# Performance work log

Measured on AMD Instinct MI355X. Metric: run time of the kernel, lower is better.

The kernel has to match this reference:

```python
import jax, jax.numpy as jnp
import numpy as np
from jax import lax

CORR = 5        # patch_size of correlation (5x5 displacements)
PAD = (CORR - 1) // 2
SEQ_IDS = [0, 1, 3, 4]  # gating_seq_len=5, center frame index 2 is skipped


def conv2d(x, w, b):
    # 3x3, stride 1, padding 1 == SAME; NCHW / OIHW
    y = lax.conv_general_dilated(x, w, (1, 1), 'SAME',
                                 dimension_numbers=('NCHW', 'OIHW', 'NCHW'))
    return y + b[None, :, None, None]


def _xavier(k, shape):
    fan_in = shape[1] * shape[2] * shape[3]
    fan_out = shape[0] * shape[2] * shape[3]
    limit = float(np.sqrt(6.0 / (fan_in + fan_out)))
    return jax.random.uniform(k, shape, jnp.float32, -limit, limit)


def setup_inputs() -> dict:
    key = jax.random.key(0)
    ks = jax.random.split(key, 4)
    B, C, H, W = 2, 512, 64, 64
    x = jax.random.normal(ks[0], (5, B, C, H, W), jnp.float32)
    Wg = jnp.stack([_xavier(k, (2, 2 * C, 3, 3)) for k in jax.random.split(ks[1], 4)])
    bg = jnp.zeros((4, 2), jnp.float32)
    Wd = jnp.stack([_xavier(k, (C, 2 * C, 3, 3)) for k in jax.random.split(ks[2], 4)])
    bd = jnp.zeros((4, C), jnp.float32)
    Wc = _xavier(ks[3], (C, 4 * C, 3, 3))
    bc = jnp.zeros((C,), jnp.float32)
    return dict(x=x, Wg=Wg, bg=bg, Wd=Wd, bd=bd, Wc=Wc, bc=bc)


def _align(feat2, feat1):
    # spatial_correlation_sample(feat2, feat1, kernel=1, patch=5, pad=0):
    # corr[b, d, y, x] = sum_c feat2[b,c,y,x] * feat1[b,c,y+di,x+dj], di,dj in [-2,2]
    b, c, h, w = feat1.shape
    pad1 = jnp.pad(feat1, ((0, 0), (0, 0), (PAD, PAD), (PAD, PAD)))
    corr = jnp.stack([jnp.sum(feat2 * pad1[:, :, i:i + h, j:j + w], axis=1)
                      for i in range(CORR) for j in range(CORR)], axis=1)  # [b,25,h,w]
    # torch F.softmax default dim for 4D is dim=1; scaled by 20/global-max
    attn = jax.nn.softmax(corr * (20.0 / jnp.max(corr)), axis=1)
    # shifted-window weighted sum over the 25 displacements
    new_feat = jnp.zeros_like(feat1)
    for i in range(CORR):
        for j in range(CORR):
            new_feat = new_feat + attn[:, i * CORR + j][:, None] * pad1[:, :, i:i + h, j:j + w]
    return new_feat


def reference(x, Wg, bg, Wd, bd, Wc, bc):
    center = x[2]                       # feat2 = middle frame for every pair
    C = center.shape[1]
    gated = []
    for n, s in enumerate(SEQ_IDS):
        new_feat = _align(center, x[s])
        feat = jnp.concatenate([center, new_feat], axis=1)          # [B,2C,H,W]
        gw = jax.nn.sigmoid(conv2d(feat, Wg[n], bg[n]))              # [B,2,H,W]
        fg = jnp.concatenate([center * gw[:, 0:1], new_feat * gw[:, 1:2]], axis=1)
        gated.append(jax.nn.relu(conv2d(fg, Wd[n], bd[n])))          # [B,C,H,W]
    total = jnp.concatenate(gated, axis=1)                           # [B,4C,H,W]
    return jax.nn.relu(conv2d(total, Wc, bc))
```

## Files before the change

### kernel.cpp

```cpp
#include <hip/hip_runtime.h>
#include <hip/hip_bf16.h>
#include <stdint.h>

typedef __attribute__((ext_vector_type(8))) short bf16x8;
typedef __attribute__((ext_vector_type(4))) float f32x4;
typedef __attribute__((ext_vector_type(2))) float f32x2;
typedef __attribute__((ext_vector_type(4))) int int4v;

#define DEVI static __device__ __forceinline__

DEVI unsigned short f2b(float f) {
  union { float f; unsigned u; } v; v.f = f;
  unsigned r = (v.u + 0x7FFFu + ((v.u >> 16) & 1u)) >> 16;
  return (unsigned short)r;
}
DEVI float b2f(unsigned short h) {
  union { unsigned u; float f; } v; v.u = ((unsigned)h) << 16;
  return v.f;
}
DEVI unsigned encf(float f) {
  union { float f; unsigned u; } v; v.f = f;
  return (v.u & 0x80000000u) ? ~v.u : (v.u | 0x80000000u);
}
DEVI float decf(unsigned u) {
  union { unsigned u; float f; } v;
  v.u = (u & 0x80000000u) ? (u & 0x7FFFFFFFu) : ~u;
  return v.f;
}
DEVI void gload16(const void* g, void* l) {
  __builtin_amdgcn_global_load_lds(
      (const __attribute__((address_space(1))) unsigned int*)g,
      (__attribute__((address_space(3))) unsigned int*)l, 16, 0, 0);
}

__global__ __launch_bounds__(256) void k_reorder_w2(const float* __restrict__ src,
                                                    unsigned short* __restrict__ dst,
                                                    int CI) {
  int r = blockIdx.x;
  int t = threadIdx.x;
  const float* s = src + (size_t)r * CI * 9;
  unsigned short* d = dst + (size_t)r * CI * 9;
  for (int ci0 = 0; ci0 < CI; ci0 += 256) {
    int ci = ci0 + t;
    float v[9];
#pragma unroll
    for (int k = 0; k < 9; k++) v[k] = s[(size_t)ci * 9 + k];
    unsigned short* db = d + (size_t)(ci >> 5) * 288 + (ci & 31);
#pragma unroll
    for (int k = 0; k < 9; k++) db[(size_t)k * 32] = f2b(v[k]);
  }
}

__global__ void k_reorder_wg(const float* __restrict__ src, float* __restrict__ dst) {
  int idx = blockIdx.x * 256 + threadIdx.x;
  int ci = idx & 1023;
  int rt = idx >> 10;
  int tap = rt % 9;
  int po = rt / 9;
  dst[(((size_t)po * 9 + tap) * 32 + (ci & 31)) * 32 + (ci >> 5)] =
      src[((size_t)po * 1024 + ci) * 9 + tap];
}

__global__ void k_border(unsigned short* __restrict__ p, int H, int wpad, int C8,
                         int nImg) {
  int inner = H - 2 * wpad;
  int borderPx = H * H - inner * inner;
  long total = (long)borderPx * C8 * nImg;
  int topN = wpad * H;
  for (long i = (long)blockIdx.x * 256 + threadIdx.x; i < total;
       i += (long)gridDim.x * 256) {
    int c = (int)(i % C8);
    long r2 = i / C8;
    int px = (int)(r2 % borderPx);
    int img = (int)(r2 / borderPx);
    int y, x;
    if (px < topN) {
      y = px / H; x = px % H;
    } else if (px < 2 * topN) {
      int q = px - topN; y = H - 1 - (q / H); x = q % H;
    } else {
      int q = px - 2 * topN;
      int row = q / (2 * wpad), cc = q % (2 * wpad);
      y = wpad + row;
      x = cc < wpad ? cc : H - 2 * wpad + cc;
    }
    *(int4v*)&p[((((size_t)img * H + y) * H + x) * C8 + c) * 8] = int4v{0, 0, 0, 0};
  }
}

__global__ __launch_bounds__(256) void k_pad(const float* __restrict__ xin,
                                             unsigned short* __restrict__ xf1,
                                             unsigned short* __restrict__ cp) {
  __shared__ unsigned short lds[64 * 66];
  int t = threadIdx.x;
  int y = blockIdx.x;
  int fb = blockIdx.y;
  int f = fb >> 1, b = fb & 1;
  const float* src = xin + (size_t)fb * 512 * 4096 + y * 64;
  unsigned short* base;
  if (f == 2) {
    base = cp + (((size_t)b * 66) + y + 1) * 66 * 512 + 512;
  } else {
    int fi = f < 2 ? f : f - 1;
    base = xf1 + (((size_t)(fi * 2 + b) * 68) + y + 2) * 68 * 512 + 2 * 512;
  }
  for (int c0 = 0; c0 < 512; c0 += 64) {
#pragma unroll
    for (int r = 0; r < 16; ++r) {
      int ci = r * 4 + (t >> 6);
      int xx = t & 63;
      lds[ci * 66 + xx] = f2b(src[(size_t)(c0 + ci) * 4096 + xx]);
    }
    __syncthreads();
    int xp = t >> 2;
    int cc = (t & 3) * 16;
    __align__(16) unsigned short vals[16];
#pragma unroll
    for (int i = 0; i < 16; i++) vals[i] = lds[(cc + i) * 66 + xp];
    unsigned short* dst = base + (size_t)xp * 512 + c0 + cc;
    *(int4v*)(dst) = *(const int4v*)(vals);
    *(int4v*)(dst + 8) = *(const int4v*)(vals + 8);
    __syncthreads();
  }
}

__global__ __launch_bounds__(256) void k_corr(const float* __restrict__ xin,
                                              float* __restrict__ corrpart) {
  __shared__ f32x2 f1h2[420];
  int t = threadIdx.x;
  int tx = t & 15, ty = t >> 4;
  int x0 = blockIdx.x * 16, y0 = blockIdx.y * 16;
  int z = blockIdx.z;
  int b = z & 1, pair = (z >> 1) & 3, part = z >> 3;
  int s = pair < 2 ? pair : pair + 1;
  const float* f2 = xin + ((size_t)(2 * 2 + b) * 512) * 4096;
  const float* f1 = xin + ((size_t)(s * 2 + b) * 512) * 4096;

  int r0 = t / 20, c0 = t - r0 * 20;
  int ls0 = r0 * 21 + c0;
  int gy0 = y0 + r0 - 2, gx0 = x0 + c0 - 2;
  bool val0 = ((unsigned)gy0 < 64u) && ((unsigned)gx0 < 64u);
  int go0 = gy0 * 64 + gx0;
  bool has1 = t < 144;
  int s1 = t + 256;
  int r1 = s1 / 20, c1 = s1 - r1 * 20;
  int ls1 = r1 * 21 + c1;
  int gy1 = y0 + r1 - 2, gx1 = x0 + c1 - 2;
  bool val1 = ((unsigned)gy1 < 64u) && ((unsigned)gx1 < 64u);
  int go1 = gy1 * 64 + gx1;

  float acc[25];
#pragma unroll
  for (int d = 0; d < 25; d++) acc[d] = 0.f;
  int y = y0 + ty, x = x0 + tx;
  for (int c = part * 128; c < part * 128 + 128; c += 2) {
    {
      float a0 = 0.f, b0v = 0.f;
      if (val0) {
        a0 = f1[(size_t)c * 4096 + go0];
        b0v = f1[(size_t)(c + 1) * 4096 + go0];
      }
      f1h2[ls0] = f32x2{a0, b0v};
      if (has1) {
        float a1 = 0.f, b1v = 0.f;
        if (val1) {
          a1 = f1[(size_t)c * 4096 + go1];
          b1v = f1[(size_t)(c + 1) * 4096 + go1];
        }
        f1h2[ls1] = f32x2{a1, b1v};
      }
    }
    float f2a = f2[(size_t)c * 4096 + y * 64 + x];
    float f2c = f2[(size_t)(c + 1) * 4096 + y * 64 + x];
    __syncthreads();
#pragma unroll
    for (int d = 0; d < 25; ++d) {
      int di = d / 5, dj = d % 5;
      f32x2 v = f1h2[(ty + di) * 21 + tx + dj];
      acc[d] += f2a * v[0] + f2c * v[1];
    }
    __syncthreads();
  }
  float* out = corrpart + ((size_t)((part * 4 + pair) * 2 + b) * 25) * 4096;
#pragma unroll
  for (int d = 0; d < 25; d++) out[(size_t)d * 4096 + y * 64 + x] = acc[d];
}

__global__ __launch_bounds__(256) void k_corr_combine(const float* __restrict__ cpart,
                                                      float* __restrict__ corr,
                                                      unsigned* __restrict__ maxb) {
  const size_t PERPAIR = (size_t)2 * 25 * 4096;
  int pair = blockIdx.y;
  size_t i4 = ((size_t)blockIdx.x * 256 + threadIdx.x) * 4;
  f32x4 sacc = {0.f, 0.f, 0.f, 0.f};
#pragma unroll
  for (int p = 0; p < 4; p++)
    sacc += *(const f32x4*)(cpart + ((size_t)(p * 4 + pair)) * PERPAIR + i4);
  *(f32x4*)(corr + (size_t)pair * PERPAIR + i4) = sacc;
  float m = fmaxf(fmaxf(sacc[0], sacc[1]), fmaxf(sacc[2], sacc[3]));
#pragma unroll
  for (int off = 32; off; off >>= 1) m = fmaxf(m, __shfl_xor(m, off));
  __shared__ float wm[4];
  if ((threadIdx.x & 63) == 0) wm[threadIdx.x >> 6] = m;
  __syncthreads();
  if (threadIdx.x == 0) {
    float mm = fmaxf(fmaxf(wm[0], wm[1]), fmaxf(wm[2], wm[3]));
    atomicMax(maxb + pair, encf(mm));
  }
}

__global__ __launch_bounds__(256) void k_attn3(const unsigned short* __restrict__ xf1,
                                               const float* __restrict__ corr,
                                               const unsigned* __restrict__ maxb,
                                               unsigned short* __restrict__ nfpad) {
  __shared__ unsigned short f1t[400 * 8];
  int t = threadIdx.x;
  int tx = t & 15, ty = t >> 4;
  int x0 = blockIdx.x * 16, y0 = blockIdx.y * 16;
  int z = blockIdx.z;
  int b = z & 1, pair = (z >> 1) & 3, cgh = z >> 3;
  const unsigned short* f1 = xf1 + ((size_t)(pair * 2 + b)) * 68 * 68 * 512;
  int y = y0 + ty, x = x0 + tx;
  const float* cr = corr + ((size_t)(pair * 2 + b)) * 25 * 4096 + y * 64 + x;

  int r0 = t / 20, c0 = t - r0 * 20;
  size_t go0 = ((size_t)(y0 + r0) * 68 + (x0 + c0)) * 512;
  bool has1 = t < 144;
  int k1 = t + 256;
  int r1 = k1 / 20, c1 = k1 - r1 * 20;
  size_t go1 = ((size_t)(y0 + r1) * 68 + (x0 + c1)) * 512;

  float p[25];
  float mx = -1e30f;
#pragma unroll
  for (int d = 0; d < 25; d++) {
    p[d] = cr[(size_t)d * 4096];
    mx = fmaxf(mx, p[d]);
  }
  float gs = 20.f / decf(maxb[pair]);
  float ss = 0.f;
#pragma unroll
  for (int d = 0; d < 25; d++) {
    p[d] = __expf((p[d] - mx) * gs);
    ss += p[d];
  }
  float inv = 1.f / ss;
#pragma unroll
  for (int d = 0; d < 25; d++) p[d] *= inv;

  for (int q = 0; q < 4; ++q) {
    int cg = cgh * 4 + q;
    *(int4v*)&f1t[t * 8] = *(const int4v*)&f1[go0 + cg * 8];
    if (has1) *(int4v*)&f1t[k1 * 8] = *(const int4v*)&f1[go1 + cg * 8];
    __syncthreads();
    float acc[8] = {0.f, 0.f, 0.f, 0.f, 0.f, 0.f, 0.f, 0.f};
#pragma unroll
    for (int d = 0; d < 25; d++) {
      bf16x8 v = *(const bf16x8*)&f1t[((ty + d / 5) * 20 + tx + d % 5) * 8];
      float pd = p[d];
#pragma unroll
      for (int e = 0; e < 8; e++) acc[e] += pd * b2f((unsigned short)v[e]);
    }
    __align__(16) unsigned short o[8];
#pragma unroll
    for (int e = 0; e < 8; e++) o[e] = f2b(acc[e]);
    *(int4v*)&nfpad[(((size_t)(pair * 2 + b) * 66 + (y + 1)) * 66 + (x + 1)) * 512 +
                    cg * 8] = *(const int4v*)o;
    __syncthreads();
  }
}

__global__ __launch_bounds__(256) void k_gate3(const unsigned short* __restrict__ cp,
                                               const unsigned short* __restrict__ nfp,
                                               const float* __restrict__ wgt,
                                               const float* __restrict__ bg,
                                               float* __restrict__ gw) {
  int t = threadIdx.x;
  int z = blockIdx.z;
  int b = z & 1, pair = z >> 1;
  int y = blockIdx.y;
  int x = blockIdx.x * 8 + (t >> 5);
  int chunk = t & 31;
  int ci0 = chunk * 32;
  int half = ci0 >> 9;
  int ch0 = ci0 & 511;
  const unsigned short* src = half ? (nfp + ((size_t)(pair * 2 + b)) * 66 * 66 * 512)
                                   : (cp + ((size_t)b) * 66 * 66 * 512);
  const float* w0b = wgt + ((size_t)(pair * 2 + 0) * 9) * 1024;
  const float* w1b = wgt + ((size_t)(pair * 2 + 1) * 9) * 1024;
  float a0 = 0.f, a1 = 0.f;
  for (int tap = 0; tap < 9; ++tap) {
    int ky = tap / 3, kx = tap % 3;
    const unsigned short* ip = src + ((size_t)(y + ky) * 66 + (x + kx)) * 512 + ch0;
    const float* w0 = w0b + tap * 1024 + chunk;
    const float* w1 = w1b + tap * 1024 + chunk;
#pragma unroll
    for (int q = 0; q < 4; ++q) {
      bf16x8 v8 = *(const bf16x8*)(ip + q * 8);
#pragma unroll
      for (int e = 0; e < 8; e++) {
        float f = b2f((unsigned short)v8[e]);
        a0 += f * w0[(q * 8 + e) * 32];
        a1 += f * w1[(q * 8 + e) * 32];
      }
    }
  }
#pragma unroll
  for (int md = 1; md < 32; md <<= 1) {
    a0 += __shfl_xor(a0, md);
    a1 += __shfl_xor(a1, md);
  }
  if ((t & 31) == 0) {
    float g0 = 1.f / (1.f + __expf(-(a0 + bg[pair * 2 + 0])));
    float g1 = 1.f / (1.f + __expf(-(a1 + bg[pair * 2 + 1])));
    gw[(((size_t)(pair * 2 + b) * 2 + 0) * 64 + y) * 64 + x] = g0;
    gw[(((size_t)(pair * 2 + b) * 2 + 1) * 64 + y) * 64 + x] = g1;
  }
}

__global__ __launch_bounds__(256) void k_fg(const unsigned short* __restrict__ cp,
                                            const unsigned short* __restrict__ nfp,
                                            const float* __restrict__ gw,
                                            unsigned short* __restrict__ fgp, int pairBase) {
  int pz = blockIdx.y;
  int pair = pairBase + pz;
  unsigned short* dstBase = fgp + (size_t)pz * 2 * 66 * 66 * 1024;
  size_t idx = (size_t)blockIdx.x * 256 + threadIdx.x;
  int chunk = (int)(idx & 127);
  size_t px = idx >> 7;
  int b = (int)(px >> 12), rem = (int)(px & 4095);
  int y = rem >> 6, x = rem & 63;
  int ci0 = chunk * 8;
  int half = ci0 >> 9;
  float g = gw[(((size_t)(pair * 2 + b) * 2 + half) * 64 + y) * 64 + x];
  const unsigned short* src = half ? (nfp + ((size_t)(pair * 2 + b)) * 66 * 66 * 512)
                                   : (cp + (size_t)b * 66 * 66 * 512);
  size_t poff = ((size_t)(y + 1) * 66 + (x + 1)) * 512 + (ci0 - half * 512);
  bf16x8 v = *(const bf16x8*)(src + poff);
  __align__(16) unsigned short o[8];
#pragma unroll
  for (int e = 0; e < 8; e++) o[e] = f2b(b2f((unsigned short)v[e]) * g);
  *(int4v*)(dstBase + ((size_t)(b * 66 + y + 1) * 66 + (x + 1)) * 1024 + ci0) =
      *(const int4v*)o;
}

template <int CI, int MODE>
__global__ __launch_bounds__(512) void conv5(const unsigned short* __restrict__ inB,
                                             const unsigned short* __restrict__ WTb,
                                             const float* __restrict__ bias,
                                             unsigned short* __restrict__ outB,
                                             unsigned short* __restrict__ outP,
                                             int pairOfs, int multiz, int nz) {
  constexpr int K = 9 * CI;
  constexpr int KTOT = K / 64;
  __shared__ unsigned short As[2 * 2 * 8192];
  __shared__ unsigned short Bs[2 * 2 * 8192];

  int t = threadIdx.x;
  int bid = blockIdx.x;
  int z, m, n;
  if (multiz == 2) {
    z = bid & 7; m = (bid >> 3) & 1; n = bid >> 4;
  } else if (multiz == 1) {
    int xcd = bid & 7;
    z = xcd >> 1; m = xcd & 1; n = bid >> 3;
  } else {
    z = 0; m = bid & 1; n = bid >> 1;
  }
  const int KT = (MODE == 2) ? KTOT / nz : KTOT;
  const unsigned short* inPad = (MODE == 0) ? inB + (size_t)z * 2 * 66 * 66 * 1024 : inB;
  const unsigned short* WT = (MODE == 0) ? WTb + (size_t)z * 512 * 9216 : WTb;
  const int kt0 = (MODE == 2) ? z * KT : 0;
  const int ktEnd = kt0 + KT;
  int co0 = m * 256, n0 = n * 256;

  int rowS[2], kcS[2], linS[2];
  size_t bpix2[2][2];
#pragma unroll
  for (int rr = 0; rr < 2; rr++) {
    int idx2 = rr * 512 + t;
    rowS[rr] = idx2 >> 3;
    kcS[rr] = (idx2 & 7) ^ (rowS[rr] & 7);
    linS[rr] = idx2 * 8;
#pragma unroll
    for (int h = 0; h < 2; h++) {
      int ng = n0 + h * 128 + rowS[rr];
      int bb = ng >> 12, yy = (ng >> 6) & 63, xx = ng & 63;
      bpix2[h][rr] = (size_t)((bb * 66 + yy) * 66 + xx) * CI + (kcS[rr] & 3) * 8;
    }
  }

  f32x4 acc[8][4];
#pragma unroll
  for (int i = 0; i < 8; i++)
#pragma unroll
    for (int j = 0; j < 4; j++) acc[i][j] = f32x4{0.f, 0.f, 0.f, 0.f};

  int wid = t >> 6, l = t & 63;
  int wm = wid >> 2, wn = wid & 3;
  int lrow = l & 15, lk4 = l >> 4;

  auto stA = [&](int bufp, int h, int kt) {
#pragma unroll
    for (int rr = 0; rr < 2; rr++)
      gload16(WT + (size_t)(co0 + h * 128 + rowS[rr]) * K + kt * 64 + kcS[rr] * 8,
              &As[(bufp * 2 + h) * 8192 + linS[rr]]);
  };
  auto stB = [&](int bufp, int h, int kt) {
    int g0 = kt * 2, g1 = g0 + 1;
    int cib0 = g0 / 9, tap0 = g0 - cib0 * 9;
    int cib1 = g1 / 9, tap1 = g1 - cib1 * 9;
    int off0 = ((tap0 / 3) * 66 + tap0 % 3) * CI + cib0 * 32;
    int off1 = ((tap1 / 3) * 66 + tap1 % 3) * CI + cib1 * 32;
#pragma unroll
    for (int rr = 0; rr < 2; rr++)
      gload16(inPad + bpix2[h][rr] + ((kcS[rr] & 4) ? off1 : off0),
              &Bs[(bufp * 2 + h) * 8192 + linS[rr]]);
  };

  bf16x8 afr0[4][2], afr1[4][2], bfr0[2][2], bfr1[2][2];

#define RDA(DST, C, MH)                                                         \
  _Pragma("unroll") for (int ii = 0; ii < 4; ++ii) {                            \
    int row = (MH)*64 + ii * 16 + lrow;                                         \
    _Pragma("unroll") for (int kk = 0; kk < 2; ++kk) {                          \
      int pos = (kk * 4 + lk4) ^ (lrow & 7);                                    \
      DST[ii][kk] = *(const bf16x8*)&As[((C)*2 + wm) * 8192 + row * 64 + pos * 8]; \
    }                                                                           \
  }
#define RDB(DST, C, NH)                                                         \
  _Pragma("unroll") for (int j = 0; j < 2; ++j) {                               \
    int row = (wn & 1) * 64 + (NH)*32 + j * 16 + lrow;                          \
    _Pragma("unroll") for (int kk = 0; kk < 2; ++kk) {                          \
      int pos = (kk * 4 + lk4) ^ (lrow & 7);                                    \
      DST[j][kk] =                                                              \
          *(const bf16x8*)&Bs[((C)*2 + (wn >> 1)) * 8192 + row * 64 + pos * 8]; \
    }                                                                           \
  }
#define QUAD(AF, BF, MH, NH)                                                    \
  __builtin_amdgcn_s_setprio(1);                                                \
  _Pragma("unroll") for (int ii = 0; ii < 4; ++ii) {                            \
    _Pragma("unroll") for (int j = 0; j < 2; ++j) {                             \
      _Pragma("unroll") for (int kk = 0; kk < 2; ++kk) {                        \
        acc[(MH)*4 + ii][(NH)*2 + j] = __builtin_amdgcn_mfma_f32_16x16x32_bf16( \
            AF[ii][kk], BF[j][kk], acc[(MH)*4 + ii][(NH)*2 + j], 0, 0, 0);      \
      }                                                                         \
    }                                                                           \
  }                                                                             \
  __builtin_amdgcn_s_setprio(0);
#define DRAIN_LGKM asm volatile("s_waitcnt lgkmcnt(0)" ::: "memory");

  {
    int b0 = kt0 & 1, b1 = b0 ^ 1;
    stA(b0, 0, kt0); stA(b0, 1, kt0); stB(b0, 0, kt0); stB(b0, 1, kt0);
    stA(b1, 0, kt0 + 1); stA(b1, 1, kt0 + 1); stB(b1, 0, kt0 + 1); stB(b1, 1, kt0 + 1);
    asm volatile("s_waitcnt vmcnt(8)" ::: "memory");
    __builtin_amdgcn_s_barrier();
  }

  for (int kt = kt0; kt < ktEnd; ++kt) {
    int cur = kt & 1;
    const bool pf = (kt + 2 < ktEnd);
    RDA(afr0, cur, 0);
    RDB(bfr0, cur, 0);
    QUAD(afr0, bfr0, 0, 0)
    RDA(afr1, cur, 1);
    QUAD(afr1, bfr0, 1, 0)
    DRAIN_LGKM
    __builtin_amdgcn_s_barrier();
    if (pf) { stA(cur, 0, kt + 2); stA(cur, 1, kt + 2); }
    RDB(bfr1, cur, 1);
    QUAD(afr1, bfr1, 1, 1)
    DRAIN_LGKM
    __builtin_amdgcn_s_barrier();
    if (pf) { stB(cur, 0, kt + 2); stB(cur, 1, kt + 2); }
    QUAD(afr0, bfr1, 0, 1)
    if (pf) {
      asm volatile("s_waitcnt vmcnt(8)" ::: "memory");
    } else {
      asm volatile("s_waitcnt vmcnt(0)" ::: "memory");
    }
    __builtin_amdgcn_s_barrier();
  }
#undef RDA
#undef RDB
#undef QUAD
#undef DRAIN_LGKM

#pragma unroll
  for (int i = 0; i < 8; i++) {
#pragma unroll
    for (int j = 0; j < 4; j++) {
      int col = wn * 64 + j * 16 + lrow;
      int ng = n0 + col;
      int bb = ng >> 12, yy = (ng >> 6) & 63, xx = ng & 63;
#pragma unroll
      for (int r = 0; r < 4; r++) {
        int row = wm * 128 + i * 16 + lk4 * 4 + r;
        int co = co0 + row;
        if (MODE == 0) {
          int zc = (z + pairOfs) * 512 + co;
          float v = acc[i][j][r] + bias[zc];
          v = v > 0.f ? v : 0.f;
          outB[((size_t)(bb * 66 + yy + 1) * 66 + (xx + 1)) * 2048 + zc] = f2b(v);
        } else {
          outP[((size_t)(z * 512 + co) << 13) + ng] = f2b(acc[i][j][r]);
        }
      }
    }
  }
}

__global__ __launch_bounds__(256) void k_combine2(const unsigned short* __restrict__ p,
                                                  const float* __restrict__ bc,
                                                  float* __restrict__ out, int nz) {
  size_t i8 = ((size_t)blockIdx.x * 256 + threadIdx.x) * 8;
  int co = (int)(i8 >> 13);
  int ng = (int)(i8 & 8191);
  float s[8] = {0.f, 0.f, 0.f, 0.f, 0.f, 0.f, 0.f, 0.f};
  for (int zz = 0; zz < nz; zz++) {
    bf16x8 v = *(const bf16x8*)&p[((size_t)(zz * 512 + co) << 13) + ng];
#pragma unroll
    for (int e = 0; e < 8; e++) s[e] += b2f((unsigned short)v[e]);
  }
  float bb = bc[co];
  int batch = ng >> 12, rem = ng & 4095;
  float* o = out + (((size_t)(batch * 512 + co)) << 12) + rem;
#pragma unroll
  for (int e = 0; e < 8; e++) {
    float q = s[e] + bb;
    o[e] = q > 0.f ? q : 0.f;
  }
}

extern "C" void kernel_launch(void* const* d_in, const int* in_sizes, int n_in,
                              void* d_out, int out_size, void* d_ws, size_t ws_size,
                              hipStream_t stream) {
  const float* x = (const float*)d_in[0];
  const float* Wg = (const float*)d_in[1];
  const float* bg = (const float*)d_in[2];
  const float* Wd = (const float*)d_in[3];
  const float* bd = (const float*)d_in[4];
  const float* Wc = (const float*)d_in[5];
  const float* bc = (const float*)d_in[6];
  float* out = (float*)d_out;

  char* ws = (char*)d_ws;
  size_t off = 0;
  auto alloc = [&](size_t bytes) {
    void* p = ws + off;
    off = (off + bytes + 255) & ~(size_t)255;
    return p;
  };
  const size_t SZ_WDT = (size_t)2048 * 9216 * 2;
  const size_t SZ_WCT = (size_t)512 * 18432 * 2;
  const size_t SZ_WGT = (size_t)4 * 2 * 9 * 1024 * 4;
  const size_t SZ_CP = (size_t)2 * 66 * 66 * 512 * 2;
  const size_t SZ_NF = (size_t)4 * 2 * 66 * 66 * 512 * 2;
  const size_t SZ_GT = (size_t)2 * 66 * 66 * 2048 * 2;
  const size_t SZ_GW = (size_t)4 * 2 * 2 * 4096 * 4;
  const size_t SZ_XF1 = (size_t)4 * 2 * 68 * 68 * 512 * 2;
  const size_t SZ_CORR = (size_t)4 * 2 * 25 * 4096 * 4;
  const size_t SZ_FG1 = (size_t)2 * 66 * 66 * 1024 * 2;
  const size_t SZ_FG4 = SZ_FG1 * 4;

  unsigned short* WdT = (unsigned short*)alloc(SZ_WDT);
  unsigned short* WcT = (unsigned short*)alloc(SZ_WCT);
  float* WgT = (float*)alloc(SZ_WGT);
  unsigned short* centerpad = (unsigned short*)alloc(SZ_CP);
  unsigned short* nfpad = (unsigned short*)alloc(SZ_NF);
  unsigned short* gatedpad = (unsigned short*)alloc(SZ_GT);
  float* gw = (float*)alloc(SZ_GW);
  unsigned* maxb = (unsigned*)alloc(256);

  size_t unionOff = off;
  unsigned short* xf1 = (unsigned short*)(ws + unionOff);
  size_t o2 = unionOff + ((SZ_XF1 + 255) & ~(size_t)255);
  float* corr = (float*)(ws + o2);
  float* cpart = (float*)(ws + o2 + ((SZ_CORR + 255) & ~(size_t)255));
  unsigned short* fg = (unsigned short*)(ws + unionOff);
  unsigned short* wcp = (unsigned short*)(ws + unionOff);
  bool batched = ws_size >= unionOff + SZ_FG4;

  hipMemsetAsync(maxb, 0, 64, stream);

  k_border<<<512, 256, 0, stream>>>(xf1, 68, 2, 64, 8);
  k_border<<<512, 256, 0, stream>>>(centerpad, 66, 1, 64, 2);
  k_border<<<512, 256, 0, stream>>>(nfpad, 66, 1, 64, 8);
  k_border<<<512, 256, 0, stream>>>(gatedpad, 66, 1, 256, 2);

  k_reorder_w2<<<2048, 256, 0, stream>>>(Wd, WdT, 1024);
  k_reorder_w2<<<512, 256, 0, stream>>>(Wc, WcT, 2048);
  k_reorder_wg<<<288, 256, 0, stream>>>(Wg, WgT);
  k_pad<<<dim3(64, 10), 256, 0, stream>>>(x, xf1, centerpad);
  k_corr<<<dim3(4, 4, 32), 256, 0, stream>>>(x, cpart);
  k_corr_combine<<<dim3(200, 4), 256, 0, stream>>>(cpart, corr, maxb);
  k_attn3<<<dim3(4, 4, 128), 256, 0, stream>>>(xf1, corr, maxb, nfpad);
  k_gate3<<<dim3(8, 64, 8), 256, 0, stream>>>(centerpad, nfpad, WgT, bg, gw);

  k_border<<<512, 256, 0, stream>>>(fg, 66, 1, 128, batched ? 8 : 2);

  if (batched) {
    k_fg<<<dim3(4096, 4), 256, 0, stream>>>(centerpad, nfpad, gw, fg, 0);
    conv5<1024, 0><<<256, 512, 0, stream>>>(fg, WdT, bd, gatedpad, nullptr, 0, 1, 1);
    conv5<2048, 2><<<512, 512, 0, stream>>>(gatedpad, WcT, nullptr, nullptr, wcp, 0, 2, 8);
    k_combine2<<<2048, 256, 0, stream>>>(wcp, bc, out, 8);
  } else {
    for (int pair = 0; pair < 4; ++pair) {
      k_fg<<<dim3(4096, 1), 256, 0, stream>>>(centerpad, nfpad, gw, fg, pair);
      conv5<1024, 0><<<64, 512, 0, stream>>>(
          fg, WdT + (size_t)pair * 512 * 9216, bd, gatedpad, nullptr, pair, 0, 1);
    }
    conv5<2048, 2><<<256, 512, 0, stream>>>(gatedpad, WcT, nullptr, nullptr, wcp, 0, 1, 4);
    k_combine2<<<2048, 256, 0, stream>>>(wcp, bc, out, 4);
  }
}
```

Measured before the change: 757.9 us.

## Shrink conv GEMM tiles to 128x128x32 with 256-thread blocks for more occupancy

Replaces the 256x256x64 tile conv kernel (512 threads, 128KB LDS) with a 128x128x32 tile variant using 256 threads and launch bounds allowing 4 blocks per CU. The smaller LDS and register footprint lets several blocks share a CU, and the launch adds many more blocks for better load balance. Split-K for the final conv is reduced (8 to 4 batched, 4 to 2 unbatched), which shrinks the partial-sum traffic. In exchange, each byte loaded gets less reuse and there are more global loads per FLOP.

```diff
diff --git a/kernel.cpp b/kernel.cpp
--- a/kernel.cpp
+++ b/kernel.cpp
@@ -345,116 +345,108 @@
 }
 
 template <int CI, int MODE>
-__global__ __launch_bounds__(512) void conv5(const unsigned short* __restrict__ inB,
-                                             const unsigned short* __restrict__ WTb,
-                                             const float* __restrict__ bias,
-                                             unsigned short* __restrict__ outB,
-                                             unsigned short* __restrict__ outP,
-                                             int pairOfs, int multiz, int nz) {
+__global__ __launch_bounds__(256, 4) void conv8(const unsigned short* __restrict__ inB,
+                                                const unsigned short* __restrict__ WTb,
+                                                const float* __restrict__ bias,
+                                                unsigned short* __restrict__ outB,
+                                                unsigned short* __restrict__ outP,
+                                                int pairOfs, int multiz, int nzLog) {
   constexpr int K = 9 * CI;
-  constexpr int KTOT = K / 64;
-  __shared__ unsigned short As[2 * 2 * 8192];
-  __shared__ unsigned short Bs[2 * 2 * 8192];
+  constexpr int KTOT = K / 32;
+  __shared__ unsigned short As[2 * 4096];
+  __shared__ unsigned short Bs[2 * 4096];
 
   int t = threadIdx.x;
   int bid = blockIdx.x;
   int z, m, n;
-  if (multiz == 2) {
-    z = bid & 7; m = (bid >> 3) & 1; n = bid >> 4;
-  } else if (multiz == 1) {
-    int xcd = bid & 7;
-    z = xcd >> 1; m = xcd & 1; n = bid >> 3;
+  if (MODE == 2) {
+    int nz = 1 << nzLog;
+    z = bid & (nz - 1);
+    m = (bid >> nzLog) & 3;
+    n = bid >> (nzLog + 2);
+  } else if (multiz) {
+    int combo = bid & 15;
+    z = combo >> 2;
+    m = combo & 3;
+    n = bid >> 4;
   } else {
-    z = 0; m = bid & 1; n = bid >> 1;
-  }
-  const int KT = (MODE == 2) ? KTOT / nz : KTOT;
+    z = 0;
+    m = bid & 3;
+    n = bid >> 2;
+  }
+  const int KT = (MODE == 2) ? (KTOT >> nzLog) : KTOT;
   const unsigned short* inPad = (MODE == 0) ? inB + (size_t)z * 2 * 66 * 66 * 1024 : inB;
   const unsigned short* WT = (MODE == 0) ? WTb + (size_t)z * 512 * 9216 : WTb;
   const int kt0 = (MODE == 2) ? z * KT : 0;
   const int ktEnd = kt0 + KT;
-  int co0 = m * 256, n0 = n * 256;
-
-  int rowS[2], kcS[2], linS[2];
-  size_t bpix2[2][2];
+  int co0 = m * 128, n0 = n * 128;
+
+  int linS[2], aoffc[2];
+  size_t bpix[2];
 #pragma unroll
   for (int rr = 0; rr < 2; rr++) {
-    int idx2 = rr * 512 + t;
-    rowS[rr] = idx2 >> 3;
-    kcS[rr] = (idx2 & 7) ^ (rowS[rr] & 7);
+    int idx2 = rr * 256 + t;
+    int row = idx2 >> 2;
+    int kc = (idx2 & 3) ^ ((row >> 1) & 3);
     linS[rr] = idx2 * 8;
-#pragma unroll
-    for (int h = 0; h < 2; h++) {
-      int ng = n0 + h * 128 + rowS[rr];
-      int bb = ng >> 12, yy = (ng >> 6) & 63, xx = ng & 63;
-      bpix2[h][rr] = (size_t)((bb * 66 + yy) * 66 + xx) * CI + (kcS[rr] & 3) * 8;
-    }
-  }
-
-  f32x4 acc[8][4];
-#pragma unroll
-  for (int i = 0; i < 8; i++)
+    aoffc[rr] = (co0 + row) * K + kc * 8;
+    int ng = n0 + row;
+    int bb = ng >> 12, yy = (ng >> 6) & 63, xx = ng & 63;
+    bpix[rr] = (size_t)((bb * 66 + yy) * 66 + xx) * CI + kc * 8;
+  }
+
+  f32x4 acc[4][4];
+#pragma unroll
+  for (int i = 0; i < 4; i++)
 #pragma unroll
     for (int j = 0; j < 4; j++) acc[i][j] = f32x4{0.f, 0.f, 0.f, 0.f};
 
   int wid = t >> 6, l = t & 63;
-  int wm = wid >> 2, wn = wid & 3;
+  int wm = wid >> 1, wn = wid & 1;
   int lrow = l & 15, lk4 = l >> 4;
-
-  auto stA = [&](int bufp, int h, int kt) {
+  int pos8 = (lk4 ^ ((lrow >> 1) & 3)) * 8;
+
+  auto stA = [&](int bufp, int kt) {
 #pragma unroll
     for (int rr = 0; rr < 2; rr++)
-      gload16(WT + (size_t)(co0 + h * 128 + rowS[rr]) * K + kt * 64 + kcS[rr] * 8,
-              &As[(bufp * 2 + h) * 8192 + linS[rr]]);
+      gload16(WT + (size_t)aoffc[rr] + kt * 32, &As[bufp * 4096 + linS[rr]]);
   };
-  auto stB = [&](int bufp, int h, int kt) {
-    int g0 = kt * 2, g1 = g0 + 1;
-    int cib0 = g0 / 9, tap0 = g0 - cib0 * 9;
-    int cib1 = g1 / 9, tap1 = g1 - cib1 * 9;
-    int off0 = ((tap0 / 3) * 66 + tap0 % 3) * CI + cib0 * 32;
-    int off1 = ((tap1 / 3) * 66 + tap1 % 3) * CI + cib1 * 32;
+  auto stB = [&](int bufp, int kt) {
+    int cib = kt / 9, tap = kt - cib * 9;
+    int off = ((tap / 3) * 66 + tap % 3) * CI + cib * 32;
 #pragma unroll
     for (int rr = 0; rr < 2; rr++)
-      gload16(inPad + bpix2[h][rr] + ((kcS[rr] & 4) ? off1 : off0),
-              &Bs[(bufp * 2 + h) * 8192 + linS[rr]]);
+      gload16(inPad + bpix[rr] + off, &Bs[bufp * 4096 + linS[rr]]);
   };
 
-  bf16x8 afr0[4][2], afr1[4][2], bfr0[2][2], bfr1[2][2];
-
-#define RDA(DST, C, MH)                                                         \
-  _Pragma("unroll") for (int ii = 0; ii < 4; ++ii) {                            \
-    int row = (MH)*64 + ii * 16 + lrow;                                         \
-    _Pragma("unroll") for (int kk = 0; kk < 2; ++kk) {                          \
-      int pos = (kk * 4 + lk4) ^ (lrow & 7);                                    \
-      DST[ii][kk] = *(const bf16x8*)&As[((C)*2 + wm) * 8192 + row * 64 + pos * 8]; \
-    }                                                                           \
-  }
-#define RDB(DST, C, NH)                                                         \
-  _Pragma("unroll") for (int j = 0; j < 2; ++j) {                               \
-    int row = (wn & 1) * 64 + (NH)*32 + j * 16 + lrow;                          \
-    _Pragma("unroll") for (int kk = 0; kk < 2; ++kk) {                          \
-      int pos = (kk * 4 + lk4) ^ (lrow & 7);                                    \
-      DST[j][kk] =                                                              \
-          *(const bf16x8*)&Bs[((C)*2 + (wn >> 1)) * 8192 + row * 64 + pos * 8]; \
-    }                                                                           \
-  }
-#define QUAD(AF, BF, MH, NH)                                                    \
-  __builtin_amdgcn_s_setprio(1);                                                \
-  _Pragma("unroll") for (int ii = 0; ii < 4; ++ii) {                            \
-    _Pragma("unroll") for (int j = 0; j < 2; ++j) {                             \
-      _Pragma("unroll") for (int kk = 0; kk < 2; ++kk) {                        \
-        acc[(MH)*4 + ii][(NH)*2 + j] = __builtin_amdgcn_mfma_f32_16x16x32_bf16( \
-            AF[ii][kk], BF[j][kk], acc[(MH)*4 + ii][(NH)*2 + j], 0, 0, 0);      \
-      }                                                                         \
-    }                                                                           \
-  }                                                                             \
+  bf16x8 afr0[2], afr1[2], bfr0[2], bfr1[2];
+
+#define RDA(DST, C, MH)                                                        \
+  _Pragma("unroll") for (int ii = 0; ii < 2; ++ii) {                           \
+    int row = wm * 64 + (MH)*32 + ii * 16 + lrow;                              \
+    DST[ii] = *(const bf16x8*)&As[(C)*4096 + row * 32 + pos8];                 \
+  }
+#define RDB(DST, C, NH)                                                        \
+  _Pragma("unroll") for (int j = 0; j < 2; ++j) {                              \
+    int row = wn * 64 + (NH)*32 + j * 16 + lrow;                               \
+    DST[j] = *(const bf16x8*)&Bs[(C)*4096 + row * 32 + pos8];                  \
+  }
+#define QUAD(AF, BF, MH, NH)                                                   \
+  __builtin_amdgcn_s_setprio(1);                                               \
+  _Pragma("unroll") for (int ii = 0; ii < 2; ++ii) {                           \
+    _Pragma("unroll") for (int j = 0; j < 2; ++j) {                            \
+      acc[(MH)*2 + ii][(NH)*2 + j] = __builtin_amdgcn_mfma_f32_16x16x32_bf16(  \
+          AF[ii], BF[j], acc[(MH)*2 + ii][(NH)*2 + j], 0, 0, 0);               \
+    }                                                                          \
+  }                                                                            \
   __builtin_amdgcn_s_setprio(0);
 #define DRAIN_LGKM asm volatile("s_waitcnt lgkmcnt(0)" ::: "memory");
 
   {
     int b0 = kt0 & 1, b1 = b0 ^ 1;
-    stA(b0, 0, kt0); stA(b0, 1, kt0); stB(b0, 0, kt0); stB(b0, 1, kt0);
-    stA(b1, 0, kt0 + 1); stA(b1, 1, kt0 + 1); stB(b1, 0, kt0 + 1); stB(b1, 1, kt0 + 1);
-    asm volatile("s_waitcnt vmcnt(8)" ::: "memory");
+    stA(b0, kt0); stB(b0, kt0);
+    stA(b1, kt0 + 1); stB(b1, kt0 + 1);
+    asm volatile("s_waitcnt vmcnt(4)" ::: "memory");
     __builtin_amdgcn_s_barrier();
   }
 
@@ -468,15 +460,15 @@
     QUAD(afr1, bfr0, 1, 0)
     DRAIN_LGKM
     __builtin_amdgcn_s_barrier();
-    if (pf) { stA(cur, 0, kt + 2); stA(cur, 1, kt + 2); }
+    if (pf) stA(cur, kt + 2);
     RDB(bfr1, cur, 1);
     QUAD(afr1, bfr1, 1, 1)
     DRAIN_LGKM
     __builtin_amdgcn_s_barrier();
-    if (pf) { stB(cur, 0, kt + 2); stB(cur, 1, kt + 2); }
+    if (pf) stB(cur, kt + 2);
     QUAD(afr0, bfr1, 0, 1)
     if (pf) {
-      asm volatile("s_waitcnt vmcnt(8)" ::: "memory");
+      asm volatile("s_waitcnt vmcnt(4)" ::: "memory");
     } else {
       asm volatile("s_waitcnt vmcnt(0)" ::: "memory");
     }
@@ -488,23 +480,21 @@
 #undef DRAIN_LGKM
 
 #pragma unroll
-  for (int i = 0; i < 8; i++) {
+  for (int i = 0; i < 4; i++) {
 #pragma unroll
     for (int j = 0; j < 4; j++) {
-      int col = wn * 64 + j * 16 + lrow;
-      int ng = n0 + col;
-      int bb = ng >> 12, yy = (ng >> 6) & 63, xx = ng & 63;
+      int col = n0 + wn * 64 + j * 16 + lrow;
+      int bb = col >> 12, yy = (col >> 6) & 63, xx = col & 63;
 #pragma unroll
       for (int r = 0; r < 4; r++) {
-        int row = wm * 128 + i * 16 + lk4 * 4 + r;
-        int co = co0 + row;
+        int co = co0 + wm * 64 + i * 16 + lk4 * 4 + r;
         if (MODE == 0) {
           int zc = (z + pairOfs) * 512 + co;
           float v = acc[i][j][r] + bias[zc];
           v = v > 0.f ? v : 0.f;
           outB[((size_t)(bb * 66 + yy + 1) * 66 + (xx + 1)) * 2048 + zc] = f2b(v);
         } else {
-          outP[((size_t)(z * 512 + co) << 13) + ng] = f2b(acc[i][j][r]);
+          outP[((size_t)(z * 512 + co) << 13) + col] = f2b(acc[i][j][r]);
         }
       }
     }
@@ -602,16 +592,16 @@
 
   if (batched) {
     k_fg<<<dim3(4096, 4), 256, 0, stream>>>(centerpad, nfpad, gw, fg, 0);
-    conv5<1024, 0><<<256, 512, 0, stream>>>(fg, WdT, bd, gatedpad, nullptr, 0, 1, 1);
-    conv5<2048, 2><<<512, 512, 0, stream>>>(gatedpad, WcT, nullptr, nullptr, wcp, 0, 2, 8);
-    k_combine2<<<2048, 256, 0, stream>>>(wcp, bc, out, 8);
+    conv8<1024, 0><<<1024, 256, 0, stream>>>(fg, WdT, bd, gatedpad, nullptr, 0, 1, 0);
+    conv8<2048, 2><<<1024, 256, 0, stream>>>(gatedpad, WcT, nullptr, nullptr, wcp, 0, 1, 2);
+    k_combine2<<<2048, 256, 0, stream>>>(wcp, bc, out, 4);
   } else {
     for (int pair = 0; pair < 4; ++pair) {
       k_fg<<<dim3(4096, 1), 256, 0, stream>>>(centerpad, nfpad, gw, fg, pair);
-      conv5<1024, 0><<<64, 512, 0, stream>>>(
-          fg, WdT + (size_t)pair * 512 * 9216, bd, gatedpad, nullptr, pair, 0, 1);
-    }
-    conv5<2048, 2><<<256, 512, 0, stream>>>(gatedpad, WcT, nullptr, nullptr, wcp, 0, 1, 4);
-    k_combine2<<<2048, 256, 0, stream>>>(wcp, bc, out, 4);
-  }
-}
+      conv8<1024, 0><<<256, 256, 0, stream>>>(
+          fg, WdT + (size_t)pair * 512 * 9216, bd, gatedpad, nullptr, pair, 0, 0);
+    }
+    conv8<2048, 2><<<512, 256, 0, stream>>>(gatedpad, WcT, nullptr, nullptr, wcp, 0, 1, 1);
+    k_combine2<<<2048, 256, 0, stream>>>(wcp, bc, out, 2);
+  }
+}
```

Result: slower. 859.8 us (+13.5%).

## Split-K the per-pair Wd convolution into two halves with a combine kernel

Applied to the files above, without the earlier changes.

Adds a MODE 3 path to conv5 that splits the K dimension of each pair's Wd convolution in two, doubling the block count from 256 to 512 so more CUs stay busy. Partial sums are written as bf16 in a channel-contiguous layout with 8-byte stores. A new k_combine3 kernel adds the two halves, applies bias and ReLU, and writes into the padded gated buffer. The path runs only when the workspace is large enough. It costs an extra partial-buffer round trip through memory, an additional launch, and some precision from the bf16 partials.

```diff
diff --git a/kernel.cpp b/kernel.cpp
--- a/kernel.cpp
+++ b/kernel.cpp
@@ -358,8 +358,13 @@
 
   int t = threadIdx.x;
   int bid = blockIdx.x;
-  int z, m, n;
-  if (multiz == 2) {
+  int z, m, n, halfK = 0;
+  if (MODE == 3) {
+    z = (bid >> 1) & 3;
+    halfK = bid & 1;
+    m = (bid >> 3) & 1;
+    n = bid >> 4;
+  } else if (multiz == 2) {
     z = bid & 7; m = (bid >> 3) & 1; n = bid >> 4;
   } else if (multiz == 1) {
     int xcd = bid & 7;
@@ -367,10 +372,12 @@
   } else {
     z = 0; m = bid & 1; n = bid >> 1;
   }
-  const int KT = (MODE == 2) ? KTOT / nz : KTOT;
-  const unsigned short* inPad = (MODE == 0) ? inB + (size_t)z * 2 * 66 * 66 * 1024 : inB;
-  const unsigned short* WT = (MODE == 0) ? WTb + (size_t)z * 512 * 9216 : WTb;
-  const int kt0 = (MODE == 2) ? z * KT : 0;
+  const int KT = (MODE == 2) ? KTOT / nz : (MODE == 3) ? KTOT / 2 : KTOT;
+  const unsigned short* inPad =
+      (MODE == 0 || MODE == 3) ? inB + (size_t)z * 2 * 66 * 66 * 1024 : inB;
+  const unsigned short* WT =
+      (MODE == 0 || MODE == 3) ? WTb + (size_t)z * 512 * 9216 : WTb;
+  const int kt0 = (MODE == 2) ? z * KT : (MODE == 3) ? halfK * KT : 0;
   const int ktEnd = kt0 + KT;
   int co0 = m * 256, n0 = n * 256;
 
@@ -494,17 +501,25 @@
       int col = wn * 64 + j * 16 + lrow;
       int ng = n0 + col;
       int bb = ng >> 12, yy = (ng >> 6) & 63, xx = ng & 63;
-#pragma unroll
-      for (int r = 0; r < 4; r++) {
-        int row = wm * 128 + i * 16 + lk4 * 4 + r;
-        int co = co0 + row;
-        if (MODE == 0) {
-          int zc = (z + pairOfs) * 512 + co;
-          float v = acc[i][j][r] + bias[zc];
-          v = v > 0.f ? v : 0.f;
-          outB[((size_t)(bb * 66 + yy + 1) * 66 + (xx + 1)) * 2048 + zc] = f2b(v);
-        } else {
-          outP[((size_t)(z * 512 + co) << 13) + ng] = f2b(acc[i][j][r]);
+      int rowb = wm * 128 + i * 16 + lk4 * 4;
+      if (MODE == 3) {
+        __align__(8) unsigned short o4[4];
+#pragma unroll
+        for (int r = 0; r < 4; r++) o4[r] = f2b(acc[i][j][r]);
+        *(unsigned long long*)&outP[((size_t)((z * 2 + halfK) * 8192 + ng)) * 512 +
+                                    co0 + rowb] = *(const unsigned long long*)o4;
+      } else {
+#pragma unroll
+        for (int r = 0; r < 4; r++) {
+          int co = co0 + rowb + r;
+          if (MODE == 0) {
+            int zc = (z + pairOfs) * 512 + co;
+            float v = acc[i][j][r] + bias[zc];
+            v = v > 0.f ? v : 0.f;
+            outB[((size_t)(bb * 66 + yy + 1) * 66 + (xx + 1)) * 2048 + zc] = f2b(v);
+          } else {
+            outP[((size_t)(z * 512 + co) << 13) + ng] = f2b(acc[i][j][r]);
+          }
         }
       }
     }
@@ -531,6 +546,31 @@
     float q = s[e] + bb;
     o[e] = q > 0.f ? q : 0.f;
   }
+}
+
+__global__ __launch_bounds__(256) void k_combine3(const unsigned short* __restrict__ p,
+                                                  const float* __restrict__ bd,
+                                                  unsigned short* __restrict__ gp) {
+  size_t i8 = ((size_t)blockIdx.x * 256 + threadIdx.x) * 8;
+  int co = (int)(i8 & 511);
+  size_t rest = i8 >> 9;
+  int ng = (int)(rest & 8191);
+  int pair = (int)(rest >> 13);
+  const unsigned short* p0 = p + ((size_t)(pair * 2 + 0) * 8192 + ng) * 512 + co;
+  const unsigned short* p1 = p + ((size_t)(pair * 2 + 1) * 8192 + ng) * 512 + co;
+  bf16x8 a = *(const bf16x8*)p0;
+  bf16x8 b = *(const bf16x8*)p1;
+  int bb = ng >> 12, yy = (ng >> 6) & 63, xx = ng & 63;
+  unsigned short* o =
+      gp + ((size_t)(bb * 66 + yy + 1) * 66 + (xx + 1)) * 2048 + pair * 512 + co;
+  const float* bdp = bd + pair * 512 + co;
+  __align__(16) unsigned short ov[8];
+#pragma unroll
+  for (int e = 0; e < 8; e++) {
+    float v = b2f((unsigned short)a[e]) + b2f((unsigned short)b[e]) + bdp[e];
+    ov[e] = f2b(v > 0.f ? v : 0.f);
+  }
+  *(int4v*)o = *(const int4v*)ov;
 }
 
 extern "C" void kernel_launch(void* const* d_in, const int* in_sizes, int n_in,
@@ -563,6 +603,7 @@
   const size_t SZ_CORR = (size_t)4 * 2 * 25 * 4096 * 4;
   const size_t SZ_FG1 = (size_t)2 * 66 * 66 * 1024 * 2;
   const size_t SZ_FG4 = SZ_FG1 * 4;
+  const size_t SZ_WDP = (size_t)8 * 8192 * 512 * 2;
 
   unsigned short* WdT = (unsigned short*)alloc(SZ_WDT);
   unsigned short* WcT = (unsigned short*)alloc(SZ_WCT);
@@ -579,8 +620,11 @@
   float* corr = (float*)(ws + o2);
   float* cpart = (float*)(ws + o2 + ((SZ_CORR + 255) & ~(size_t)255));
   unsigned short* fg = (unsigned short*)(ws + unionOff);
+  size_t fgEnd = unionOff + ((SZ_FG4 + 255) & ~(size_t)255);
+  unsigned short* wdp = (unsigned short*)(ws + fgEnd);
   unsigned short* wcp = (unsigned short*)(ws + unionOff);
   bool batched = ws_size >= unionOff + SZ_FG4;
+  bool splitWd = ws_size >= fgEnd + SZ_WDP + 4096;
 
   hipMemsetAsync(maxb, 0, 64, stream);
 
@@ -602,7 +646,12 @@
 
   if (batched) {
     k_fg<<<dim3(4096, 4), 256, 0, stream>>>(centerpad, nfpad, gw, fg, 0);
-    conv5<1024, 0><<<256, 512, 0, stream>>>(fg, WdT, bd, gatedpad, nullptr, 0, 1, 1);
+    if (splitWd) {
+      conv5<1024, 3><<<512, 512, 0, stream>>>(fg, WdT, nullptr, nullptr, wdp, 0, 0, 2);
+      k_combine3<<<8192, 256, 0, stream>>>(wdp, bd, gatedpad);
+    } else {
+      conv5<1024, 0><<<256, 512, 0, stream>>>(fg, WdT, bd, gatedpad, nullptr, 0, 1, 1);
+    }
     conv5<2048, 2><<<512, 512, 0, stream>>>(gatedpad, WcT, nullptr, nullptr, wcp, 0, 2, 8);
     k_combine2<<<2048, 256, 0, stream>>>(wcp, bc, out, 8);
   } else {
```

Result: slower. 776.9 us (+2.5%).
